# Kernel tuning notes

Measured on AMD Instinct MI355X. Metric: run time of the kernel, lower is better.

The kernel has to match this reference:

```python
import jax, jax.numpy as jnp
import numpy as np

B, S, H, DK = 64, 8192, 8, 8  # d_k must equal n_wires=8 (encoder maps feature i -> RX on wire i)
E = H * DK                    # embed_dim = 64


def _quantum_heads(x, theta):
    """Exact closed form of the 8-wire circuit per (batch, token, head).

    Circuit: RX(x_i) then trainable RX(theta_i) on each wire i (RX(a)RX(b)=RX(a+b)),
    CNOT chain (0->1, 1->2, ..., 6->7, 7->0), then <Z_w> on every wire.
    Starting from |0..0>, the post-RX state is a product state with per-wire
    bit probabilities p(1)=sin^2(a_i/2); CNOTs classically permute basis states:
    bit_k' = XOR(b_0..b_k) for k>=1 and bit_0' = XOR(b_1..b_7). Since the bits are
    independent with E[(-1)^{b_j}] = cos(a_j):
        <Z_0> = prod_{j=1..7} cos(a_j)
        <Z_k> = prod_{j=0..k} cos(a_j)   (k >= 1)
    This equals the full statevector simulation exactly.
    """
    a = x.reshape(B, S, H, DK) + theta            # angles, [B,S,H,8]
    c = jnp.cos(a)
    cp = jnp.cumprod(c, axis=-1)                  # <Z_k> for k>=1 is cp[..., k]
    z0 = jnp.prod(c[..., 1:], axis=-1, keepdims=True)
    return jnp.concatenate([z0, cp[..., 1:]], axis=-1)  # [B,S,H,8]


def setup_inputs() -> dict:
    key = jax.random.key(0)
    k1, k2, k3, k4 = jax.random.split(key, 4)
    lim = 1.0 / float(np.sqrt(E))
    return {
        "x": jax.random.normal(k1, (B, S, E), jnp.float32),
        "theta": jax.random.normal(k2, (DK,), jnp.float32),
        "w_combine": jax.random.uniform(k3, (E, E), jnp.float32, -lim, lim),
        "b_combine": jax.random.uniform(k4, (E,), jnp.float32, -lim, lim),
    }


def reference(x, theta, w_combine, b_combine):
    # q, k, v are all the SAME quantum projection of the SAME x in the original.
    z = _quantum_heads(x, theta)                              # [B,S,H,DK]
    # torch matmul on [B,S,H,DK]: attention is across the HEAD axis per token.
    scores = jnp.einsum('bshd,bstd->bsht', z, z) * (DK ** -0.5)
    attn = jax.nn.softmax(scores, axis=-1)                    # dropout: eval mode (identity)
    out = jnp.einsum('bsht,bstd->bshd', attn, z)              # [B,S,H,DK]
    # matches torch .transpose(1,2).contiguous().view(B, -1, E)
    out = out.transpose(0, 2, 1, 3).reshape(B, S, E)
    return out @ w_combine.T + b_combine
```

## Files before the change

kernel.cpp:

```cpp
#include <hip/hip_runtime.h>

typedef __attribute__((ext_vector_type(8))) short bf16x8;
typedef __attribute__((ext_vector_type(4))) float f32x4;
typedef __attribute__((ext_vector_type(2))) float f32x2;

__device__ __forceinline__ f32x2 fma2(f32x2 a, f32x2 b, f32x2 c) {
    return __builtin_elementwise_fma(a, b, c);
}

template <int CTRL>
__device__ __forceinline__ float qperm(float x) {
    return __builtin_bit_cast(float,
        __builtin_amdgcn_update_dpp(0, __builtin_bit_cast(int, x), CTRL, 0xf, 0xf, true));
}
template <int CTRL>
__device__ __forceinline__ f32x2 qperm2(f32x2 x) {
    f32x2 r;
    r.x = qperm<CTRL>(x.x);
    r.y = qperm<CTRL>(x.y);
    return r;
}

__global__ __launch_bounds__(256) void qattn(const float* __restrict__ x,
                                             const float* __restrict__ theta,
                                             const float* __restrict__ wc,
                                             const float* __restrict__ bc,
                                             float* __restrict__ out)
{
    __shared__ __align__(16) unsigned short sWhi[512 * 8];
    __shared__ __align__(16) unsigned short sWlo[512 * 8];

    const float KAPPA = 0.71419161f;
    const float INVK  = 1.40018590f;
    const float INV2PI = 0.15915494309189535f;

    const int tid = threadIdx.x;
    #pragma unroll
    for (int f0 = 0; f0 < 2; ++f0) {
        const int f = tid * 2 + f0;
        const int snt = f >> 6, ln = f & 63;
        const int s = snt >> 2, nt = snt & 3;
        const int r = nt * 16 + (ln & 15);
        const int koff = s * 32 + (ln >> 4) * 8;
        const float* wp = wc + r * 64 + koff;
        float w8[8];
        *(float4*)(&w8[0]) = *(const float4*)(wp);
        *(float4*)(&w8[4]) = *(const float4*)(wp + 4);
        #pragma unroll
        for (int j = 0; j < 8; ++j) {
            float w = w8[j] * INVK;
            unsigned u = __builtin_bit_cast(unsigned, w);
            sWhi[f * 8 + j] = (unsigned short)(u >> 16);
            float rhi = __builtin_bit_cast(float, u & 0xffff0000u);
            unsigned l = __builtin_bit_cast(unsigned, w - rhi);
            sWlo[f * 8 + j] = (unsigned short)(l >> 16);
        }
    }
    __syncthreads();

    const int lane = tid & 63;
    const int wid  = tid >> 6;
    const int h    = lane & 7;
    const int G1   = (lane >> 3) & 1;
    const int kch  = lane >> 4;
    const int col  = lane & 15;
    const int fby  = lane * 8;

    f32x2 th2p[4];
    #pragma unroll
    for (int j = 0; j < 4; ++j) {
        th2p[j].x = theta[2 * j] * INV2PI;
        th2p[j].y = theta[2 * j + 1] * INV2PI;
    }
    float bs[4];
    #pragma unroll
    for (int nt = 0; nt < 4; ++nt) bs[nt] = bc[nt * 16 + col];

    const int P = (int)blockIdx.x * 4 + wid;
    const float* xp0 = x + ((size_t)((2 * P + G1) * 8 + kch)) * 64 + h * 8;

    float4 xv[4];
    xv[0] = *(const float4*)(xp0);
    xv[1] = *(const float4*)(xp0 + 4);
    xv[2] = *(const float4*)(xp0 + 256);
    xv[3] = *(const float4*)(xp0 + 260);

    bf16x8 ahi[2], alo[2];
    #pragma unroll
    for (int s = 0; s < 2; ++s) {
        const f32x2* v2 = (const f32x2*)&xv[s * 2];
        f32x2 inv2 = {INV2PI, INV2PI};
        float c[8];
        #pragma unroll
        for (int j = 0; j < 4; ++j) {
            f32x2 a2 = fma2(v2[j], inv2, th2p[j]);
            c[2 * j]     = __builtin_amdgcn_cosf(__builtin_amdgcn_fractf(a2.x));
            c[2 * j + 1] = __builtin_amdgcn_cosf(__builtin_amdgcn_fractf(a2.y));
        }
        c[1] *= KAPPA;

        float z[8];
        z[1] = c[0] * c[1];
        #pragma unroll
        for (int d = 2; d < 8; ++d) z[d] = z[d - 1] * c[d];
        float p = c[1];
        #pragma unroll
        for (int d = 2; d < 8; ++d) p *= c[d];
        z[0] = p;

        f32x2 z2[4];
        #pragma unroll
        for (int j = 0; j < 4; ++j) { z2[j].x = z[2 * j]; z2[j].y = z[2 * j + 1]; }

        f32x2 z72[4];
        #pragma unroll
        for (int j = 0; j < 4; ++j) z72[j] = qperm2<0x141>(z2[j]);

        f32x2 osum2[4];
        #pragma unroll
        for (int j = 0; j < 4; ++j) osum2[j] = (f32x2){0.f, 0.f};
        float esum = 0.f;

        #define QSTEP(ZT)                                                      \
            do {                                                               \
                f32x2 s2 = (ZT)[0] * z2[0];                                    \
                s2 = fma2((ZT)[1], z2[1], s2);                                 \
                s2 = fma2((ZT)[2], z2[2], s2);                                 \
                s2 = fma2((ZT)[3], z2[3], s2);                                 \
                float e = __builtin_amdgcn_exp2f(s2.x + s2.y);                 \
                esum += e;                                                     \
                f32x2 e2 = {e, e};                                             \
                _Pragma("unroll")                                              \
                for (int j = 0; j < 4; ++j)                                    \
                    osum2[j] = fma2(e2, (ZT)[j], osum2[j]);                    \
            } while (0)

        QSTEP(z2);
        {
            f32x2 w2[4];
            #pragma unroll
            for (int j = 0; j < 4; ++j) w2[j] = qperm2<0xB1>(z2[j]);
            QSTEP(w2);
            #pragma unroll
            for (int j = 0; j < 4; ++j) w2[j] = qperm2<0x4E>(z2[j]);
            QSTEP(w2);
            #pragma unroll
            for (int j = 0; j < 4; ++j) w2[j] = qperm2<0x1B>(z2[j]);
            QSTEP(w2);
        }
        QSTEP(z72);
        {
            f32x2 w2[4];
            #pragma unroll
            for (int j = 0; j < 4; ++j) w2[j] = qperm2<0xB1>(z72[j]);
            QSTEP(w2);
            #pragma unroll
            for (int j = 0; j < 4; ++j) w2[j] = qperm2<0x4E>(z72[j]);
            QSTEP(w2);
            #pragma unroll
            for (int j = 0; j < 4; ++j) w2[j] = qperm2<0x1B>(z72[j]);
            QSTEP(w2);
        }
        #undef QSTEP

        float r = __builtin_amdgcn_rcpf(esum);
        f32x2 r2 = {r, r};
        f32x2 o2[4];
        #pragma unroll
        for (int j = 0; j < 4; ++j) o2[j] = osum2[j] * r2;

        unsigned hp[4], lp[4];
        #pragma unroll
        for (int pq = 0; pq < 4; ++pq) {
            unsigned e0 = __builtin_bit_cast(unsigned, o2[pq].x);
            unsigned e1 = __builtin_bit_cast(unsigned, o2[pq].y);
            hp[pq] = (e0 >> 16) | (e1 & 0xffff0000u);
            float r0 = __builtin_bit_cast(float, e0 & 0xffff0000u);
            float r1 = __builtin_bit_cast(float, e1 & 0xffff0000u);
            unsigned l0 = __builtin_bit_cast(unsigned, o2[pq].x - r0);
            unsigned l1 = __builtin_bit_cast(unsigned, o2[pq].y - r1);
            lp[pq] = (l0 >> 16) | (l1 & 0xffff0000u);
        }
        ahi[s] = __builtin_bit_cast(bf16x8, *(const unsigned(*)[4])hp);
        alo[s] = __builtin_bit_cast(bf16x8, *(const unsigned(*)[4])lp);
    }

    f32x4 acc[4];
    #pragma unroll
    for (int nt = 0; nt < 4; ++nt) acc[nt] = (f32x4){0.f, 0.f, 0.f, 0.f};
    #pragma unroll
    for (int nt = 0; nt < 4; ++nt) {
        #pragma unroll
        for (int s = 0; s < 2; ++s) {
            const int off = (s * 4 + nt) * 512 + fby;
            bf16x8 bhi = *(const bf16x8*)(&sWhi[off]);
            bf16x8 blo = *(const bf16x8*)(&sWlo[off]);
            acc[nt] = __builtin_amdgcn_mfma_f32_16x16x32_bf16(ahi[s], bhi, acc[nt], 0, 0, 0);
            acc[nt] = __builtin_amdgcn_mfma_f32_16x16x32_bf16(alo[s], bhi, acc[nt], 0, 0, 0);
            acc[nt] = __builtin_amdgcn_mfma_f32_16x16x32_bf16(ahi[s], blo, acc[nt], 0, 0, 0);
        }
    }

    #pragma unroll
    for (int q = 0; q < 4; ++q) {
        const int r16 = kch * 4 + q;
        const int hh = r16 & 7;
        const int gg = r16 >> 3;
        const int gf2 = 2 * P + gg;
        const int orow = (gf2 >> 10) * 8192 + hh * 1024 + (gf2 & 1023);
        float* op = out + orow * 64 + col;
        #pragma unroll
        for (int nt = 0; nt < 4; ++nt)
            op[nt * 16] = acc[nt][q] + bs[nt];
    }
}

extern "C" void kernel_launch(void* const* d_in, const int* in_sizes, int n_in,
                              void* d_out, int out_size, void* d_ws, size_t ws_size,
                              hipStream_t stream) {
    const float* x     = (const float*)d_in[0];
    const float* theta = (const float*)d_in[1];
    const float* wc    = (const float*)d_in[2];
    const float* bc    = (const float*)d_in[3];
    float* out = (float*)d_out;
    qattn<<<dim3(8192), dim3(256), 0, stream>>>(x, theta, wc, bc, out);
}
```

Measured before the change: 56.03 us.

## Precompute split-bf16 weights in a prep kernel and load them into registers

A one-block prep kernel now does the bf16 hi/lo split of the combine weights once and writes the result to workspace. The main kernel loses its shared-memory staging and barrier: each single-wave block loads its weight fragments straight from global (L2-resident) memory into registers. Blocks shrink from 256 to 64 threads and the grid grows fourfold. The gain is that per-block weight conversion and the __syncthreads go away; the cost is an extra kernel launch, more VGPRs for the held weight fragments, and repeated global loads of the same 16 KB by every wave.

Measured after the change: 55.65 us. About the same (-0.7%).

```diff
diff --git a/kernel.cpp b/kernel.cpp
--- a/kernel.cpp
+++ b/kernel.cpp
@@ -21,62 +21,45 @@
     return r;
 }
 
-__global__ __launch_bounds__(256) void qattn(const float* __restrict__ x,
-                                             const float* __restrict__ theta,
-                                             const float* __restrict__ wc,
-                                             const float* __restrict__ bc,
-                                             float* __restrict__ out)
+#define KAPPA 0.71419161f
+#define INVK  1.40018590f
+#define INV2PI 0.15915494309189535f
+
+__global__ __launch_bounds__(512) void prepw(const float* __restrict__ wc,
+                                             unsigned short* __restrict__ ws) {
+    const int f = threadIdx.x;
+    const int snt = f >> 6, ln = f & 63;
+    const int s = snt >> 2, nt = snt & 3;
+    const int r = nt * 16 + (ln & 15);
+    const int koff = s * 32 + (ln >> 4) * 8;
+    const float* wp = wc + r * 64 + koff;
+    float w8[8];
+    *(float4*)(&w8[0]) = *(const float4*)(wp);
+    *(float4*)(&w8[4]) = *(const float4*)(wp + 4);
+    #pragma unroll
+    for (int j = 0; j < 8; ++j) {
+        float w = w8[j] * INVK;
+        unsigned u = __builtin_bit_cast(unsigned, w);
+        ws[f * 8 + j] = (unsigned short)(u >> 16);
+        float rhi = __builtin_bit_cast(float, u & 0xffff0000u);
+        unsigned l = __builtin_bit_cast(unsigned, w - rhi);
+        ws[4096 + f * 8 + j] = (unsigned short)(l >> 16);
+    }
+}
+
+__global__ __launch_bounds__(64) void qattn(const float* __restrict__ x,
+                                            const float* __restrict__ theta,
+                                            const unsigned short* __restrict__ ws,
+                                            const float* __restrict__ bc,
+                                            float* __restrict__ out)
 {
-    __shared__ __align__(16) unsigned short sWhi[512 * 8];
-    __shared__ __align__(16) unsigned short sWlo[512 * 8];
-
-    const float KAPPA = 0.71419161f;
-    const float INVK  = 1.40018590f;
-    const float INV2PI = 0.15915494309189535f;
-
-    const int tid = threadIdx.x;
-    #pragma unroll
-    for (int f0 = 0; f0 < 2; ++f0) {
-        const int f = tid * 2 + f0;
-        const int snt = f >> 6, ln = f & 63;
-        const int s = snt >> 2, nt = snt & 3;
-        const int r = nt * 16 + (ln & 15);
-        const int koff = s * 32 + (ln >> 4) * 8;
-        const float* wp = wc + r * 64 + koff;
-        float w8[8];
-        *(float4*)(&w8[0]) = *(const float4*)(wp);
-        *(float4*)(&w8[4]) = *(const float4*)(wp + 4);
-        #pragma unroll
-        for (int j = 0; j < 8; ++j) {
-            float w = w8[j] * INVK;
-            unsigned u = __builtin_bit_cast(unsigned, w);
-            sWhi[f * 8 + j] = (unsigned short)(u >> 16);
-            float rhi = __builtin_bit_cast(float, u & 0xffff0000u);
-            unsigned l = __builtin_bit_cast(unsigned, w - rhi);
-            sWlo[f * 8 + j] = (unsigned short)(l >> 16);
-        }
-    }
-    __syncthreads();
-
-    const int lane = tid & 63;
-    const int wid  = tid >> 6;
+    const int lane = threadIdx.x;
     const int h    = lane & 7;
     const int G1   = (lane >> 3) & 1;
     const int kch  = lane >> 4;
     const int col  = lane & 15;
-    const int fby  = lane * 8;
-
-    f32x2 th2p[4];
-    #pragma unroll
-    for (int j = 0; j < 4; ++j) {
-        th2p[j].x = theta[2 * j] * INV2PI;
-        th2p[j].y = theta[2 * j + 1] * INV2PI;
-    }
-    float bs[4];
-    #pragma unroll
-    for (int nt = 0; nt < 4; ++nt) bs[nt] = bc[nt * 16 + col];
-
-    const int P = (int)blockIdx.x * 4 + wid;
+
+    const int P = (int)blockIdx.x;
     const float* xp0 = x + ((size_t)((2 * P + G1) * 8 + kch)) * 64 + h * 8;
 
     float4 xv[4];
@@ -84,6 +67,24 @@
     xv[1] = *(const float4*)(xp0 + 4);
     xv[2] = *(const float4*)(xp0 + 256);
     xv[3] = *(const float4*)(xp0 + 260);
+
+    const char* wsb = (const char*)ws;
+    bf16x8 Whi[8], Wlo[8];
+    #pragma unroll
+    for (int snt = 0; snt < 8; ++snt) {
+        Whi[snt] = *(const bf16x8*)(wsb + snt * 1024 + lane * 16);
+        Wlo[snt] = *(const bf16x8*)(wsb + 8192 + snt * 1024 + lane * 16);
+    }
+
+    f32x2 th2p[4];
+    #pragma unroll
+    for (int j = 0; j < 4; ++j) {
+        th2p[j].x = theta[2 * j] * INV2PI;
+        th2p[j].y = theta[2 * j + 1] * INV2PI;
+    }
+    float bs[4];
+    #pragma unroll
+    for (int nt = 0; nt < 4; ++nt) bs[nt] = bc[nt * 16 + col];
 
     bf16x8 ahi[2], alo[2];
     #pragma unroll
@@ -192,12 +193,10 @@
     for (int nt = 0; nt < 4; ++nt) {
         #pragma unroll
         for (int s = 0; s < 2; ++s) {
-            const int off = (s * 4 + nt) * 512 + fby;
-            bf16x8 bhi = *(const bf16x8*)(&sWhi[off]);
-            bf16x8 blo = *(const bf16x8*)(&sWlo[off]);
-            acc[nt] = __builtin_amdgcn_mfma_f32_16x16x32_bf16(ahi[s], bhi, acc[nt], 0, 0, 0);
-            acc[nt] = __builtin_amdgcn_mfma_f32_16x16x32_bf16(alo[s], bhi, acc[nt], 0, 0, 0);
-            acc[nt] = __builtin_amdgcn_mfma_f32_16x16x32_bf16(ahi[s], blo, acc[nt], 0, 0, 0);
+            const int snt = s * 4 + nt;
+            acc[nt] = __builtin_amdgcn_mfma_f32_16x16x32_bf16(ahi[s], Whi[snt], acc[nt], 0, 0, 0);
+            acc[nt] = __builtin_amdgcn_mfma_f32_16x16x32_bf16(alo[s], Whi[snt], acc[nt], 0, 0, 0);
+            acc[nt] = __builtin_amdgcn_mfma_f32_16x16x32_bf16(ahi[s], Wlo[snt], acc[nt], 0, 0, 0);
         }
     }
 
@@ -223,5 +222,7 @@
     const float* wc    = (const float*)d_in[2];
     const float* bc    = (const float*)d_in[3];
     float* out = (float*)d_out;
-    qattn<<<dim3(8192), dim3(256), 0, stream>>>(x, theta, wc, bc, out);
-}
+    unsigned short* ws = (unsigned short*)d_ws;
+    prepw<<<dim3(1), dim3(512), 0, stream>>>(wc, ws);
+    qattn<<<dim3(32768), dim3(64), 0, stream>>>(x, theta, ws, bc, out);
+}
```
